# Performance work log

Hardware: AMD Instinct MI355X
Metric: run time of the kernel (lower is better)

## Reference

```python
import jax, jax.numpy as jnp
import numpy as np


def setup_inputs() -> dict:
    key = jax.random.key(0)
    ks = jax.random.split(key, 8)
    B, N, C = 4, 2048, 1024
    H, hd, lr, R = 16, 64, 20, 200  # R = low_rank * rank_multi
    s = lambda k, shape, fan: jax.random.normal(k, shape, jnp.float32) / np.sqrt(fan)
    return {
        'x': jax.random.normal(ks[0], (B, N, C), jnp.float32),
        'qk_w': s(ks[1], (2 * C, C), C),
        'proj_w': s(ks[2], (C, C), C),
        'proj_b': jnp.zeros((C,), jnp.float32),
        'we': s(ks[3], (H, R, lr), R),
        'wr': s(ks[4], (H, R, lr), R),
        'cw_w': s(ks[5], (hd, 2 * lr), 2 * lr),
        'cw_b': jnp.zeros((hd,), jnp.float32),
    }


def _l2norm(v, eps=1e-12):
    # matches F.normalize(p=2, dim=-1): x / max(||x||, eps)
    n = jnp.sqrt(jnp.sum(v * v, axis=-1, keepdims=True))
    return v / jnp.maximum(n, eps)


def reference(x, qk_w, proj_w, proj_b, we, wr, cw_w, cw_b):
    B, N, C = x.shape
    H, R, lr = we.shape  # heads, subsample len, low_rank
    hd = C // H
    # qk projection -> q,k: [B,H,N,hd]
    qk = (x @ qk_w.T).reshape(B, N, 2, H, hd).transpose(2, 0, 3, 1, 4)
    q, k = qk[0], qk[1]
    # gen_weights: subsample N positions (embed_len > low_rank*rank_multi branch)
    idx = np.linspace(0, N - 1, R).astype(np.int64)  # static, trunc like torch
    xh = x.transpose(0, 2, 1).reshape(B, H, hd, N)[:, :, :, idx]  # [B,H,hd,R]
    we_b = jnp.einsum('bhdr,hre->bhde', xh, we)  # [B,H,hd,lr]
    wr_b = jnp.einsum('bhdr,hre->bhde', xh, wr)
    # feature map + low-rank scores
    q = _l2norm(q)
    k = _l2norm(k)
    escore = jnp.einsum('bhnd,bhde->bhne', q, we_b)  # [B,H,N,lr]
    rscore = jnp.einsum('bhnd,bhde->bhne', k, wr_b)
    score = jnp.concatenate([escore, rscore], axis=-1)  # [B,H,N,2lr]
    attn = score @ cw_w.T + cw_b  # [B,H,N,hd]
    attn = attn.transpose(0, 2, 1, 3).reshape(B, N, C)
    out = attn @ proj_w.T + proj_b  # dropout is identity at eval
    return out
```

## Files before the change

### kernel.cpp

```cpp
#include <hip/hip_runtime.h>
#include <hip/hip_bf16.h>

constexpr int B_  = 4;
constexpr int N_  = 2048;
constexpr int C_  = 1024;
constexpr int H_  = 16;
constexpr int HD  = 64;
constexpr int LR  = 20;
constexpr int RS  = 200;
constexpr int RP  = 224;

typedef __attribute__((ext_vector_type(8))) short bf16x8;
typedef __attribute__((ext_vector_type(4))) float f32x4;

__device__ __forceinline__ float b2f_raw(unsigned short u) {
    union { unsigned int i; float f; } v;
    v.i = ((unsigned int)u) << 16;
    return v.f;
}
__device__ __forceinline__ unsigned short f2b(float f) {
    __hip_bfloat16 h = __float2bfloat16(f);
    return *(unsigned short*)&h;
}
template <bool BF>
__device__ __forceinline__ float ldg(const void* p, size_t i) {
    if constexpr (BF) return b2f_raw(((const unsigned short*)p)[i]);
    else              return ((const float*)p)[i];
}

__device__ __forceinline__ void async_load16(const unsigned short* g, unsigned short* l) {
    __builtin_amdgcn_global_load_lds(
        (const __attribute__((address_space(1))) unsigned int*)(const void*)g,
        (__attribute__((address_space(3))) unsigned int*)(void*)l,
        16, 0, 0);
}

__global__ __launch_bounds__(256)
void detect_kernel(const unsigned int* __restrict__ x, int* __restrict__ flag) {
    const int t = threadIdx.x;
    int cnt = 0;
    for (int i = t; i < 1024; i += 256) {
        const unsigned int w = x[i];
        const unsigned int e = (w >> 7) & 0xFFu;
        cnt += (e >= 103u && e <= 140u) ? 1 : 0;
    }
    __shared__ int s[256];
    s[t] = cnt;
    __syncthreads();
    for (int off = 128; off > 0; off >>= 1) {
        if (t < off) s[t] += s[t + off];
        __syncthreads();
    }
    if (t == 0) *flag = (s[0] > 512) ? 1 : 0;
}

struct CvtArgs {
    const void* src[5];
    unsigned short* dst[5];
    int size[5];
};

template <bool BF>
__device__ void wec_body(const void* __restrict__ we_raw,
                         const void* __restrict__ wr_raw,
                         const void* __restrict__ cw_raw,
                         unsigned short* __restrict__ wect,
                         unsigned short* __restrict__ wrct) {
    const int o = blockIdx.x * 256 + threadIdx.x;
    if (o >= H_ * HD * RP) return;
    const int r    = o % RP;
    const int dout = (o / RP) % HD;
    const int h    = o / (RP * HD);
    float sq = 0.f, sk = 0.f;
    if (r < RS) {
        #pragma unroll
        for (int e = 0; e < LR; ++e) {
            const float cq = ldg<BF>(cw_raw, dout * 2 * LR + e);
            const float ck = ldg<BF>(cw_raw, dout * 2 * LR + LR + e);
            sq += ldg<BF>(we_raw, ((size_t)h * RS + r) * LR + e) * cq;
            sk += ldg<BF>(wr_raw, ((size_t)h * RS + r) * LR + e) * ck;
        }
    }
    wect[o] = f2b(sq);
    wrct[o] = f2b(sk);
}

template <bool BF>
__device__ void gather_body(const void* __restrict__ x_raw,
                            unsigned short* __restrict__ xh) {
    const int bh = blockIdx.x;
    if (bh >= B_ * H_) return;
    const int b = bh >> 4;
    const int h = bh & 15;
    for (int o = threadIdx.x; o < HD * RP; o += 256) {
        const int din = o & 63;
        const int r   = o >> 6;
        unsigned short v = 0;
        if (r < RS) {
            const int ir = (r * (N_ - 1)) / (RS - 1);
            const size_t idx = ((size_t)b * N_ + ir) * C_ + h * HD + din;
            if constexpr (BF) v = ((const unsigned short*)x_raw)[idx];
            else              v = f2b(((const float*)x_raw)[idx]);
        }
        xh[(size_t)bh * HD * RP + (size_t)din * RP + r] = v;
    }
}

__global__ __launch_bounds__(256)
void fused_prep_kernel(const int* __restrict__ flag, CvtArgs args,
                       const void* __restrict__ we_raw,
                       const void* __restrict__ wr_raw,
                       const void* __restrict__ cw_raw,
                       unsigned short* __restrict__ wect,
                       unsigned short* __restrict__ wrct,
                       unsigned short* __restrict__ xh) {
    const bool isbf = (*flag != 0);
    const int y = blockIdx.y;
    if (y < 5) {
        const int n4 = args.size[y] >> 2;
        const int stride = gridDim.x * blockDim.x;
        for (int i = blockIdx.x * blockDim.x + threadIdx.x; i < n4; i += stride) {
            ushort4 o;
            if (isbf) {
                o = ((const ushort4*)args.src[y])[i];
            } else {
                const float4 v = ((const float4*)args.src[y])[i];
                o.x = f2b(v.x); o.y = f2b(v.y); o.z = f2b(v.z); o.w = f2b(v.w);
            }
            ((ushort4*)args.dst[y])[i] = o;
        }
    } else if (y == 5) {
        if (isbf) wec_body<true>(we_raw, wr_raw, cw_raw, wect, wrct);
        else      wec_body<false>(we_raw, wr_raw, cw_raw, wect, wrct);
    } else {
        if (isbf) gather_body<true>(args.src[0], xh);
        else      gather_body<false>(args.src[0], xh);
    }
}

__global__ __launch_bounds__(64)
void collapse_kernel(const unsigned short* __restrict__ xh,
                     const unsigned short* __restrict__ wect,
                     const unsigned short* __restrict__ wrct,
                     unsigned short* __restrict__ we2t,
                     unsigned short* __restrict__ wr2t) {
    const int blk = blockIdx.x;
    const int bh  = blk >> 2;
    const int qk  = (blk >> 1) & 1;
    const int dh  = blk & 1;
    const int h   = bh & 15;
    const int lane = threadIdx.x;
    const int lq = lane >> 4;
    const int lm = lane & 15;

    const unsigned short* wsrc = (qk ? wrct : wect) + (size_t)h * HD * RP;
    const unsigned short* xsrc = xh + (size_t)bh * HD * RP;
    unsigned short* dst = (qk ? wr2t : we2t) + (size_t)bh * HD * HD;

    f32x4 acc[2][4];
    #pragma unroll
    for (int i = 0; i < 2; ++i)
        #pragma unroll
        for (int j = 0; j < 4; ++j) acc[i][j] = 0.f;

    for (int ks = 0; ks < RP / 32; ++ks) {
        bf16x8 a[2], bfr[4];
        #pragma unroll
        for (int rt = 0; rt < 2; ++rt)
            a[rt] = *(const bf16x8*)&wsrc[(size_t)(dh * 32 + rt * 16 + lm) * RP + ks * 32 + lq * 8];
        #pragma unroll
        for (int j = 0; j < 4; ++j)
            bfr[j] = *(const bf16x8*)&xsrc[(size_t)(j * 16 + lm) * RP + ks * 32 + lq * 8];
        #pragma unroll
        for (int rt = 0; rt < 2; ++rt)
            #pragma unroll
            for (int j = 0; j < 4; ++j)
                acc[rt][j] = __builtin_amdgcn_mfma_f32_16x16x32_bf16(
                    a[rt], bfr[j], acc[rt][j], 0, 0, 0);
    }

    #pragma unroll
    for (int rt = 0; rt < 2; ++rt)
        #pragma unroll
        for (int j = 0; j < 4; ++j)
            #pragma unroll
            for (int r = 0; r < 4; ++r) {
                const int dout = dh * 32 + rt * 16 + lq * 4 + r;
                const int din  = j * 16 + lm;
                dst[dout * HD + din] = f2b(acc[rt][j][r]);
            }
}

__global__ __launch_bounds__(256, 2)
void gemm1_score_kernel(const unsigned short* __restrict__ xb,
                        const unsigned short* __restrict__ qkwb,
                        const unsigned short* __restrict__ we2t,
                        const unsigned short* __restrict__ wr2t,
                        const unsigned short* __restrict__ cwbb,
                        unsigned short* __restrict__ attn) {
    constexpr int QS = 72;
    __shared__ __align__(16) unsigned short pool[32768];
    unsigned short* const AsBase = pool;
    unsigned short* const BsBase = pool + 16384;
    unsigned short* qn = pool;
    unsigned short* kn = pool + 128 * QS;

    const int t    = threadIdx.x;
    const int wave = t >> 6;
    const int lane = t & 63;
    const int h    = blockIdx.x;
    const int m0   = blockIdx.y * 128;
    const int K    = C_;

    const int srow  = lane >> 3;
    const int sunit = (lane & 7) ^ srow;
    const unsigned short* gA = xb + (size_t)(m0 + wave * 32 + srow) * K + sunit * 8;
    const int vb = wave * 32;
    const size_t brow = (vb < 64) ? (size_t)(h * HD + vb)
                                  : (size_t)(C_ + h * HD + (vb - 64));
    const unsigned short* gB = qkwb + (brow + srow) * K + sunit * 8;

    const int wr = (wave >> 1) * 64;
    const int wc = (wave & 1) * 64;
    const int lq = lane >> 4;
    const int lm = lane & 15;
    const int c0 = (lq ^ (lm & 7)) * 8;

    f32x4 acc[4][4];
    #pragma unroll
    for (int i = 0; i < 4; ++i)
        #pragma unroll
        for (int j = 0; j < 4; ++j) acc[i][j] = 0.f;

    auto stage = [&](int buf) {
        unsigned short* dA = AsBase + buf * 8192 + wave * 2048;
        unsigned short* dB = BsBase + buf * 8192 + wave * 2048;
        #pragma unroll
        for (int i = 0; i < 4; ++i) {
            async_load16(gA + (size_t)i * 8 * K, dA + i * 512);
            async_load16(gB + (size_t)i * 8 * K, dB + i * 512);
        }
        gA += 64; gB += 64;
    };
    auto compute = [&](int buf) {
        const unsigned short* As = AsBase + buf * 8192;
        const unsigned short* Bs = BsBase + buf * 8192;
        #pragma unroll
        for (int ks = 0; ks < 2; ++ks) {
            const int cc = c0 ^ (ks * 32);
            bf16x8 af[4], bfr[4];
            #pragma unroll
            for (int i = 0; i < 4; ++i)
                af[i] = *(const bf16x8*)&As[(wr + i * 16 + lm) * 64 + cc];
            #pragma unroll
            for (int j = 0; j < 4; ++j)
                bfr[j] = *(const bf16x8*)&Bs[(wc + j * 16 + lm) * 64 + cc];
            #pragma unroll
            for (int i = 0; i < 4; ++i)
                #pragma unroll
                for (int j = 0; j < 4; ++j)
                    acc[i][j] = __builtin_amdgcn_mfma_f32_16x16x32_bf16(
                        af[i], bfr[j], acc[i][j], 0, 0, 0);
        }
    };

    constexpr int NTK = C_ / 64;
    stage(0);
    __syncthreads();
    for (int kt = 0; kt < NTK - 1; ++kt) {
        stage((kt + 1) & 1);
        compute(kt & 1);
        __syncthreads();
    }
    compute((NTK - 1) & 1);
    __syncthreads();

    unsigned short* dst = (wc == 0) ? qn : kn;
    #pragma unroll
    for (int i = 0; i < 4; ++i) {
        float inv[4];
        #pragma unroll
        for (int r = 0; r < 4; ++r) {
            float s = 0.f;
            #pragma unroll
            for (int j = 0; j < 4; ++j) s += acc[i][j][r] * acc[i][j][r];
            s += __shfl_xor(s, 1, 64);
            s += __shfl_xor(s, 2, 64);
            s += __shfl_xor(s, 4, 64);
            s += __shfl_xor(s, 8, 64);
            inv[r] = 1.f / fmaxf(sqrtf(s), 1e-12f);
        }
        #pragma unroll
        for (int j = 0; j < 4; ++j)
            #pragma unroll
            for (int r = 0; r < 4; ++r) {
                const int row = wr + i * 16 + lq * 4 + r;
                dst[row * QS + j * 16 + lm] = f2b(acc[i][j][r] * inv[r]);
            }
    }
    __syncthreads();

    const int b  = blockIdx.y >> 4;
    const int bh = b * H_ + h;
    const unsigned short* wq = we2t + (size_t)bh * HD * HD;
    const unsigned short* wk = wr2t + (size_t)bh * HD * HD;

    bf16x8 bq[2][4], bk[2][4];
    #pragma unroll
    for (int t2 = 0; t2 < 2; ++t2)
        #pragma unroll
        for (int j = 0; j < 4; ++j) {
            const int dout = j * 16 + lm;
            bq[t2][j] = *(const bf16x8*)&wq[dout * HD + t2 * 32 + lq * 8];
            bk[t2][j] = *(const bf16x8*)&wk[dout * HD + t2 * 32 + lq * 8];
        }

    f32x4 accS[2][4];
    #pragma unroll
    for (int rt = 0; rt < 2; ++rt)
        #pragma unroll
        for (int j = 0; j < 4; ++j) accS[rt][j] = 0.f;

    #pragma unroll
    for (int rt = 0; rt < 2; ++rt) {
        const int lr = wave * 32 + rt * 16 + lm;
        bf16x8 aq0 = *(const bf16x8*)&qn[lr * QS + lq * 8];
        bf16x8 aq1 = *(const bf16x8*)&qn[lr * QS + 32 + lq * 8];
        bf16x8 ak0 = *(const bf16x8*)&kn[lr * QS + lq * 8];
        bf16x8 ak1 = *(const bf16x8*)&kn[lr * QS + 32 + lq * 8];
        #pragma unroll
        for (int j = 0; j < 4; ++j) {
            accS[rt][j] = __builtin_amdgcn_mfma_f32_16x16x32_bf16(aq0, bq[0][j], accS[rt][j], 0, 0, 0);
            accS[rt][j] = __builtin_amdgcn_mfma_f32_16x16x32_bf16(aq1, bq[1][j], accS[rt][j], 0, 0, 0);
            accS[rt][j] = __builtin_amdgcn_mfma_f32_16x16x32_bf16(ak0, bk[0][j], accS[rt][j], 0, 0, 0);
            accS[rt][j] = __builtin_amdgcn_mfma_f32_16x16x32_bf16(ak1, bk[1][j], accS[rt][j], 0, 0, 0);
        }
    }

    #pragma unroll
    for (int rt = 0; rt < 2; ++rt)
        #pragma unroll
        for (int j = 0; j < 4; ++j) {
            const int dout = j * 16 + lm;
            const float bv = b2f_raw(cwbb[dout]);
            #pragma unroll
            for (int r = 0; r < 4; ++r) {
                const int row = m0 + wave * 32 + rt * 16 + lq * 4 + r;
                attn[(size_t)row * C_ + h * HD + dout] = f2b(accS[rt][j][r] + bv);
            }
        }
}

template <bool OBF>
__device__ void mfma_gemm_body64(const unsigned short* __restrict__ A,
                                 const unsigned short* __restrict__ W,
                                 const unsigned short* __restrict__ bias,
                                 void* __restrict__ out,
                                 int M, int N, int K) {
    __shared__ __align__(16) unsigned short AsBase[16384];
    __shared__ __align__(16) unsigned short BsBase[16384];

    const int t    = threadIdx.x;
    const int wave = t >> 6;
    const int lane = t & 63;
    const int m0   = blockIdx.y * 128;
    const int n0   = blockIdx.x * 128;

    const int srow  = lane >> 3;
    const int sunit = (lane & 7) ^ srow;
    const unsigned short* gA = A + (size_t)(m0 + wave * 32 + srow) * K + sunit * 8;
    const unsigned short* gB = W + (size_t)(n0 + wave * 32 + srow) * K + sunit * 8;

    const int wr = (wave >> 1) * 64;
    const int wc = (wave & 1) * 64;
    const int lq = lane >> 4;
    const int lm = lane & 15;
    const int c0 = (lq ^ (lm & 7)) * 8;

    f32x4 acc[4][4];
    #pragma unroll
    for (int i = 0; i < 4; ++i)
        #pragma unroll
        for (int j = 0; j < 4; ++j) acc[i][j] = 0.f;

    auto stage = [&](int buf) {
        unsigned short* dA = AsBase + buf * 8192 + wave * 2048;
        unsigned short* dB = BsBase + buf * 8192 + wave * 2048;
        #pragma unroll
        for (int i = 0; i < 4; ++i) {
            async_load16(gA + (size_t)i * 8 * K, dA + i * 512);
            async_load16(gB + (size_t)i * 8 * K, dB + i * 512);
        }
        gA += 64; gB += 64;
    };
    auto compute = [&](int buf) {
        const unsigned short* As = AsBase + buf * 8192;
        const unsigned short* Bs = BsBase + buf * 8192;
        #pragma unroll
        for (int ks = 0; ks < 2; ++ks) {
            const int cc = c0 ^ (ks * 32);
            bf16x8 af[4], bfr[4];
            #pragma unroll
            for (int i = 0; i < 4; ++i)
                af[i] = *(const bf16x8*)&As[(wr + i * 16 + lm) * 64 + cc];
            #pragma unroll
            for (int j = 0; j < 4; ++j)
                bfr[j] = *(const bf16x8*)&Bs[(wc + j * 16 + lm) * 64 + cc];
            #pragma unroll
            for (int i = 0; i < 4; ++i)
                #pragma unroll
                for (int j = 0; j < 4; ++j)
                    acc[i][j] = __builtin_amdgcn_mfma_f32_16x16x32_bf16(
                        af[i], bfr[j], acc[i][j], 0, 0, 0);
        }
    };

    const int NTK = K / 64;
    stage(0);
    __syncthreads();
    for (int kt = 0; kt < NTK - 1; ++kt) {
        stage((kt + 1) & 1);
        compute(kt & 1);
        __syncthreads();
    }
    compute((NTK - 1) & 1);

    #pragma unroll
    for (int i = 0; i < 4; ++i) {
        #pragma unroll
        for (int j = 0; j < 4; ++j) {
            const int col = n0 + wc + j * 16 + lm;
            const float bv = b2f_raw(bias[col]);
            #pragma unroll
            for (int r = 0; r < 4; ++r) {
                const int row = m0 + wr + i * 16 + lq * 4 + r;
                const float v = acc[i][j][r] + bv;
                if constexpr (OBF)
                    ((__hip_bfloat16*)out)[(size_t)row * N + col] = __float2bfloat16(v);
                else
                    ((float*)out)[(size_t)row * N + col] = v;
            }
        }
    }
}

__global__ __launch_bounds__(256, 2)
void gemm2_kernel(const int* __restrict__ flag,
                  const unsigned short* __restrict__ attn,
                  const unsigned short* __restrict__ pwb,
                  const unsigned short* __restrict__ pbb,
                  void* __restrict__ out) {
    if (*flag) mfma_gemm_body64<true>(attn, pwb, pbb, out, B_ * N_, C_, C_);
    else       mfma_gemm_body64<false>(attn, pwb, pbb, out, B_ * N_, C_, C_);
}

extern "C" void kernel_launch(void* const* d_in, const int* in_sizes, int n_in,
                              void* d_out, int out_size, void* d_ws, size_t ws_size,
                              hipStream_t stream) {
    (void)in_sizes; (void)n_in; (void)out_size; (void)ws_size;

    char* ws = (char*)d_ws;
    size_t off = 0;
    auto alloc = [&](size_t bytes) {
        char* p = ws + off;
        off += (bytes + 255) & ~(size_t)255;
        return p;
    };

    int* flag = (int*)alloc(16);
    unsigned short* xb    = (unsigned short*)alloc((size_t)B_ * N_ * C_ * 2);
    unsigned short* qkwb  = (unsigned short*)alloc((size_t)2 * C_ * C_ * 2);
    unsigned short* pwb   = (unsigned short*)alloc((size_t)C_ * C_ * 2);
    unsigned short* pbb   = (unsigned short*)alloc((size_t)C_ * 2);
    unsigned short* cwbb  = (unsigned short*)alloc((size_t)HD * 2);
    unsigned short* attn  = (unsigned short*)alloc((size_t)B_ * N_ * C_ * 2);
    unsigned short* we2t  = (unsigned short*)alloc((size_t)B_ * H_ * HD * HD * 2);
    unsigned short* wr2t  = (unsigned short*)alloc((size_t)B_ * H_ * HD * HD * 2);
    unsigned short* wect  = (unsigned short*)alloc((size_t)H_ * HD * RP * 2);
    unsigned short* wrct  = (unsigned short*)alloc((size_t)H_ * HD * RP * 2);
    unsigned short* xh    = (unsigned short*)alloc((size_t)B_ * H_ * HD * RP * 2);

    const int M = B_ * N_;

    detect_kernel<<<1, 256, 0, stream>>>((const unsigned int*)d_in[0], flag);

    CvtArgs ca;
    ca.src[0] = d_in[0]; ca.dst[0] = xb;   ca.size[0] = B_ * N_ * C_;
    ca.src[1] = d_in[1]; ca.dst[1] = qkwb; ca.size[1] = 2 * C_ * C_;
    ca.src[2] = d_in[2]; ca.dst[2] = pwb;  ca.size[2] = C_ * C_;
    ca.src[3] = d_in[3]; ca.dst[3] = pbb;  ca.size[3] = C_;
    ca.src[4] = d_in[7]; ca.dst[4] = cwbb; ca.size[4] = HD;
    fused_prep_kernel<<<dim3(2048, 7), 256, 0, stream>>>(
        flag, ca, d_in[4], d_in[5], d_in[6], wect, wrct, xh);

    collapse_kernel<<<B_ * H_ * 4, 64, 0, stream>>>(xh, wect, wrct, we2t, wr2t);

    gemm1_score_kernel<<<dim3(H_, M / 128), 256, 0, stream>>>(
        xb, qkwb, we2t, wr2t, cwbb, attn);

    gemm2_kernel<<<dim3(C_ / 128, M / 128), 256, 0, stream>>>(
        flag, attn, pwb, pbb, d_out);
}
```

Baseline: 220.1 us.

## Inline dtype detection per block and remap GEMM blocks for XCD L2 locality

Removes the separate detect kernel and recomputes the bf16/fp32 detection inside each kernel with a wave shuffle reduction. For bf16 inputs it skips the conversion copy and reads the raw buffers directly. GEMM block indices are remapped so that consecutive blocks scheduled on the same XCD share row tiles, which should improve L2 reuse. The cost is redundant detection loads in every block.

```diff
diff --git a/kernel.cpp b/kernel.cpp
--- a/kernel.cpp
+++ b/kernel.cpp
@@ -35,23 +35,18 @@
         16, 0, 0);
 }
 
-__global__ __launch_bounds__(256)
-void detect_kernel(const unsigned int* __restrict__ x, int* __restrict__ flag) {
-    const int t = threadIdx.x;
+__device__ __forceinline__ bool detect_bf16(const unsigned int* __restrict__ x) {
+    const int lane = threadIdx.x & 63;
     int cnt = 0;
-    for (int i = t; i < 1024; i += 256) {
-        const unsigned int w = x[i];
+    #pragma unroll
+    for (int i = 0; i < 16; ++i) {
+        const unsigned int w = x[lane * 16 + i];
         const unsigned int e = (w >> 7) & 0xFFu;
         cnt += (e >= 103u && e <= 140u) ? 1 : 0;
     }
-    __shared__ int s[256];
-    s[t] = cnt;
-    __syncthreads();
-    for (int off = 128; off > 0; off >>= 1) {
-        if (t < off) s[t] += s[t + off];
-        __syncthreads();
-    }
-    if (t == 0) *flag = (s[0] > 512) ? 1 : 0;
+    #pragma unroll
+    for (int s = 1; s < 64; s <<= 1) cnt += __shfl_xor(cnt, s, 64);
+    return cnt > 512;
 }
 
 struct CvtArgs {
@@ -107,26 +102,23 @@
 }
 
 __global__ __launch_bounds__(256)
-void fused_prep_kernel(const int* __restrict__ flag, CvtArgs args,
+void fused_prep_kernel(CvtArgs args,
                        const void* __restrict__ we_raw,
                        const void* __restrict__ wr_raw,
                        const void* __restrict__ cw_raw,
                        unsigned short* __restrict__ wect,
                        unsigned short* __restrict__ wrct,
                        unsigned short* __restrict__ xh) {
-    const bool isbf = (*flag != 0);
+    const bool isbf = detect_bf16((const unsigned int*)args.src[0]);
     const int y = blockIdx.y;
     if (y < 5) {
+        if (isbf) return;
         const int n4 = args.size[y] >> 2;
         const int stride = gridDim.x * blockDim.x;
         for (int i = blockIdx.x * blockDim.x + threadIdx.x; i < n4; i += stride) {
+            const float4 v = ((const float4*)args.src[y])[i];
             ushort4 o;
-            if (isbf) {
-                o = ((const ushort4*)args.src[y])[i];
-            } else {
-                const float4 v = ((const float4*)args.src[y])[i];
-                o.x = f2b(v.x); o.y = f2b(v.y); o.z = f2b(v.z); o.w = f2b(v.w);
-            }
+            o.x = f2b(v.x); o.y = f2b(v.y); o.z = f2b(v.z); o.w = f2b(v.w);
             ((ushort4*)args.dst[y])[i] = o;
         }
     } else if (y == 5) {
@@ -192,11 +184,14 @@
 }
 
 __global__ __launch_bounds__(256, 2)
-void gemm1_score_kernel(const unsigned short* __restrict__ xb,
+void gemm1_score_kernel(const void* __restrict__ x_raw,
+                        const void* __restrict__ qkw_raw,
+                        const void* __restrict__ cwb_raw,
+                        const unsigned short* __restrict__ xb,
                         const unsigned short* __restrict__ qkwb,
+                        const unsigned short* __restrict__ cwbb,
                         const unsigned short* __restrict__ we2t,
                         const unsigned short* __restrict__ wr2t,
-                        const unsigned short* __restrict__ cwbb,
                         unsigned short* __restrict__ attn) {
     constexpr int QS = 72;
     __shared__ __align__(16) unsigned short pool[32768];
@@ -205,20 +200,28 @@
     unsigned short* qn = pool;
     unsigned short* kn = pool + 128 * QS;
 
+    const bool isbf = detect_bf16((const unsigned int*)x_raw);
+    const unsigned short* xs  = isbf ? (const unsigned short*)x_raw   : xb;
+    const unsigned short* qks = isbf ? (const unsigned short*)qkw_raw : qkwb;
+    const unsigned short* cwb = isbf ? (const unsigned short*)cwb_raw : cwbb;
+
     const int t    = threadIdx.x;
     const int wave = t >> 6;
     const int lane = t & 63;
-    const int h    = blockIdx.x;
-    const int m0   = blockIdx.y * 128;
-    const int K    = C_;
+    const int lin     = blockIdx.y * 16 + blockIdx.x;
+    const int logical = (lin & 7) * 128 + (lin >> 3);
+    const int h       = logical & 15;
+    const int mt      = logical >> 4;
+    const int m0      = mt * 128;
+    const int K       = C_;
 
     const int srow  = lane >> 3;
     const int sunit = (lane & 7) ^ srow;
-    const unsigned short* gA = xb + (size_t)(m0 + wave * 32 + srow) * K + sunit * 8;
+    const unsigned short* gA = xs + (size_t)(m0 + wave * 32 + srow) * K + sunit * 8;
     const int vb = wave * 32;
     const size_t brow = (vb < 64) ? (size_t)(h * HD + vb)
                                   : (size_t)(C_ + h * HD + (vb - 64));
-    const unsigned short* gB = qkwb + (brow + srow) * K + sunit * 8;
+    const unsigned short* gB = qks + (brow + srow) * K + sunit * 8;
 
     const int wr = (wave >> 1) * 64;
     const int wc = (wave & 1) * 64;
@@ -300,7 +303,7 @@
     }
     __syncthreads();
 
-    const int b  = blockIdx.y >> 4;
+    const int b  = mt >> 4;
     const int bh = b * H_ + h;
     const unsigned short* wq = we2t + (size_t)bh * HD * HD;
     const unsigned short* wk = wr2t + (size_t)bh * HD * HD;
@@ -342,7 +345,7 @@
         #pragma unroll
         for (int j = 0; j < 4; ++j) {
             const int dout = j * 16 + lm;
-            const float bv = b2f_raw(cwbb[dout]);
+            const float bv = b2f_raw(cwb[dout]);
             #pragma unroll
             for (int r = 0; r < 4; ++r) {
                 const int row = m0 + wave * 32 + rt * 16 + lq * 4 + r;
@@ -356,15 +359,13 @@
                                  const unsigned short* __restrict__ W,
                                  const unsigned short* __restrict__ bias,
                                  void* __restrict__ out,
-                                 int M, int N, int K) {
+                                 int M, int N, int K, int m0, int n0) {
     __shared__ __align__(16) unsigned short AsBase[16384];
     __shared__ __align__(16) unsigned short BsBase[16384];
 
     const int t    = threadIdx.x;
     const int wave = t >> 6;
     const int lane = t & 63;
-    const int m0   = blockIdx.y * 128;
-    const int n0   = blockIdx.x * 128;
 
     const int srow  = lane >> 3;
     const int sunit = (lane & 7) ^ srow;
@@ -445,13 +446,22 @@
 }
 
 __global__ __launch_bounds__(256, 2)
-void gemm2_kernel(const int* __restrict__ flag,
+void gemm2_kernel(const void* __restrict__ x_raw,
+                  const void* __restrict__ pw_raw,
+                  const void* __restrict__ pb_raw,
                   const unsigned short* __restrict__ attn,
                   const unsigned short* __restrict__ pwb,
                   const unsigned short* __restrict__ pbb,
                   void* __restrict__ out) {
-    if (*flag) mfma_gemm_body64<true>(attn, pwb, pbb, out, B_ * N_, C_, C_);
-    else       mfma_gemm_body64<false>(attn, pwb, pbb, out, B_ * N_, C_, C_);
+    const bool isbf = detect_bf16((const unsigned int*)x_raw);
+    const unsigned short* W = isbf ? (const unsigned short*)pw_raw : pwb;
+    const unsigned short* bias = isbf ? (const unsigned short*)pb_raw : pbb;
+    const int lin     = blockIdx.y * 8 + blockIdx.x;
+    const int logical = (lin & 7) * 64 + (lin >> 3);
+    const int n0      = (logical & 7) * 128;
+    const int m0      = (logical >> 3) * 128;
+    if (isbf) mfma_gemm_body64<true>(attn, W, bias, out, B_ * N_, C_, C_, m0, n0);
+    else      mfma_gemm_body64<false>(attn, W, bias, out, B_ * N_, C_, C_, m0, n0);
 }
 
 extern "C" void kernel_launch(void* const* d_in, const int* in_sizes, int n_in,
@@ -467,7 +477,6 @@
         return p;
     };
 
-    int* flag = (int*)alloc(16);
     unsigned short* xb    = (unsigned short*)alloc((size_t)B_ * N_ * C_ * 2);
     unsigned short* qkwb  = (unsigned short*)alloc((size_t)2 * C_ * C_ * 2);
     unsigned short* pwb   = (unsigned short*)alloc((size_t)C_ * C_ * 2);
@@ -482,8 +491,6 @@
 
     const int M = B_ * N_;
 
-    detect_kernel<<<1, 256, 0, stream>>>((const unsigned int*)d_in[0], flag);
-
     CvtArgs ca;
     ca.src[0] = d_in[0]; ca.dst[0] = xb;   ca.size[0] = B_ * N_ * C_;
     ca.src[1] = d_in[1]; ca.dst[1] = qkwb; ca.size[1] = 2 * C_ * C_;
@@ -491,13 +498,13 @@
     ca.src[3] = d_in[3]; ca.dst[3] = pbb;  ca.size[3] = C_;
     ca.src[4] = d_in[7]; ca.dst[4] = cwbb; ca.size[4] = HD;
     fused_prep_kernel<<<dim3(2048, 7), 256, 0, stream>>>(
-        flag, ca, d_in[4], d_in[5], d_in[6], wect, wrct, xh);
+        ca, d_in[4], d_in[5], d_in[6], wect, wrct, xh);
 
     collapse_kernel<<<B_ * H_ * 4, 64, 0, stream>>>(xh, wect, wrct, we2t, wr2t);
 
-    gemm1_score_kernel<<<dim3(H_, M / 128), 256, 0, stream>>>(
-        xb, qkwb, we2t, wr2t, cwbb, attn);
+    gemm1_score_kernel<<<dim3(16, M / 128), 256, 0, stream>>>(
+        d_in[0], d_in[1], d_in[7], xb, qkwb, cwbb, we2t, wr2t, attn);
 
     gemm2_kernel<<<dim3(C_ / 128, M / 128), 256, 0, stream>>>(
-        flag, attn, pwb, pbb, d_out);
-}
+        d_in[0], d_in[2], d_in[3], attn, pwb, pbb, d_out);
+}
```

After: 229.1 us. +4.1%, slower.
